# Optimization experiments

Hardware: AMD Instinct MI355X
Metric: run time of the kernel (lower is better)

The kernel has to match this reference:

```python
import math
import jax, jax.numpy as jnp
import numpy as np

N_HEAD = 16
N_EMBD = 1024
HEAD_DIM = N_EMBD // N_HEAD  # 64
SHARED = 16
PRIV = HEAD_DIM - SHARED     # 48
B, T = 4, 2048
STD = 0.02


def setup_inputs() -> dict:
    key = jax.random.key(0)
    ks = jax.random.split(key, 6)
    x = jax.random.normal(ks[0], (B, T, N_EMBD), dtype=jnp.float32)
    # Linear params stored as (in, out); bias zeros per _reset_parameters
    W_share = jax.random.normal(ks[1], (N_EMBD, SHARED), dtype=jnp.float32) * STD
    Wq = jax.random.normal(ks[2], (N_EMBD, N_HEAD * PRIV), dtype=jnp.float32) * STD
    Wk = jax.random.normal(ks[3], (N_EMBD, N_HEAD * PRIV), dtype=jnp.float32) * STD
    Wv = jax.random.normal(ks[4], (N_EMBD, N_EMBD), dtype=jnp.float32) * STD
    Wo = jax.random.normal(ks[5], (N_EMBD, N_EMBD), dtype=jnp.float32) * STD
    return {
        'hidden_states': x,
        'W_share': W_share, 'b_share': jnp.zeros((SHARED,), jnp.float32),
        'Wq': Wq, 'bq': jnp.zeros((N_HEAD * PRIV,), jnp.float32),
        'Wk': Wk, 'bk': jnp.zeros((N_HEAD * PRIV,), jnp.float32),
        'Wv': Wv, 'bv': jnp.zeros((N_EMBD,), jnp.float32),
        'Wo': Wo, 'bo': jnp.zeros((N_EMBD,), jnp.float32),
    }


def reference(hidden_states, W_share, b_share, Wq, bq, Wk, bk, Wv, bv, Wo, bo):
    x = hidden_states
    Bt, Tt, C = x.shape
    # shared projection, broadcast across heads: (B,T,s) -> (B,H,T,s)
    share = x @ W_share + b_share
    share_h = jnp.broadcast_to(share[:, None, :, :], (Bt, N_HEAD, Tt, SHARED))
    # private q/k: (B,T,H*p) -> (B,H,T,p)
    q_priv = (x @ Wq + bq).reshape(Bt, Tt, N_HEAD, PRIV).transpose(0, 2, 1, 3)
    k_priv = (x @ Wk + bk).reshape(Bt, Tt, N_HEAD, PRIV).transpose(0, 2, 1, 3)
    q = jnp.concatenate([share_h, q_priv], axis=-1)  # (B,H,T,head_dim)
    k = jnp.concatenate([share_h, k_priv], axis=-1)
    v = (x @ Wv + bv).reshape(Bt, Tt, N_HEAD, HEAD_DIM).transpose(0, 2, 1, 3)
    scale = 1.0 / math.sqrt(HEAD_DIM)
    att = jnp.einsum('bhqd,bhkd->bhqk', q, k) * scale
    causal = jnp.tril(jnp.ones((Tt, Tt), dtype=bool))
    att = jnp.where(causal[None, None, :, :], att, -jnp.inf)
    att = jax.nn.softmax(att, axis=-1)
    y = jnp.einsum('bhqk,bhkd->bhqd', att, v)
    y = y.transpose(0, 2, 1, 3).reshape(Bt, Tt, C)
    y = y @ Wo + bo
    return y
```

## Files before the change

kernel.cpp:

```cpp
#include <hip/hip_runtime.h>
#include <hip/hip_bf16.h>

typedef unsigned short u16;
typedef short short8 __attribute__((ext_vector_type(8)));
typedef float f32x4 __attribute__((ext_vector_type(4)));

#define N_EMBD   1024
#define N_HEADS  16
#define HEAD_DIM 64
#define PRIV     48
#define SEQ_T    2048
#define BATCH    4
#define M_ROWS   (BATCH*SEQ_T)
#define PNS      2816
#define NTILES   (SEQ_T/64)
#define NT_K     16

#if __has_builtin(__builtin_amdgcn_exp2f)
#define EXP2(x) __builtin_amdgcn_exp2f(x)
#else
#define EXP2(x) exp2f(x)
#endif

#if __has_builtin(__builtin_amdgcn_global_load_lds)
#define HAVE_GLL 1
#else
#define HAVE_GLL 0
#endif

__device__ __forceinline__ u16 f2bf(float f) {
  __hip_bfloat16 h = __float2bfloat16(f);
  return *reinterpret_cast<u16*>(&h);
}
__device__ __forceinline__ float bf2f(u16 s) {
  __hip_bfloat16 h;
  *reinterpret_cast<u16*>(&h) = s;
  return __bfloat162float(h);
}
__device__ __forceinline__ float loadv(const void* p, size_t i, int isf32) {
  return isf32 ? ((const float*)p)[i] : bf2f(((const u16*)p)[i]);
}
__device__ __forceinline__ u16 truncbf(float f) {
  unsigned u = __builtin_bit_cast(unsigned, f);
  return (u16)(u >> 16);
}
#if HAVE_GLL
__device__ __forceinline__ void gload_lds16(const u16* g, u16* l) {
  __builtin_amdgcn_global_load_lds(
      (const __attribute__((address_space(1))) void*)g,
      (__attribute__((address_space(3))) void*)l, 16, 0, 0);
}
#endif

__global__ __launch_bounds__(256) void detect_kernel(const u16* __restrict__ x,
                                                     int* __restrict__ flag) {
  __shared__ int cnt;
  if (threadIdx.x == 0) cnt = 0;
  __syncthreads();
  u16 v = x[2 * threadIdx.x];
  int e = (v >> 7) & 0xFF;
  int junk = (e >= 0xC0 || (e != 0 && e <= 0x30)) ? 1 : 0;
  if (junk) atomicAdd(&cnt, 1);
  __syncthreads();
  if (threadIdx.x == 0) *flag = (cnt > 16) ? 1 : 0;
}

__global__ __launch_bounds__(256) void pack_t_kernel(
    const void* __restrict__ Wsh, const void* __restrict__ Wq,
    const void* __restrict__ Wk,  const void* __restrict__ Wv,
    const void* __restrict__ Wo,
    const void* __restrict__ bsh, const void* __restrict__ bq,
    const void* __restrict__ bk,  const void* __restrict__ bv,
    const void* __restrict__ bo,
    u16* __restrict__ Wcat, u16* __restrict__ Woc,
    u16* __restrict__ bcat, u16* __restrict__ boc,
    const int* __restrict__ flagp)
{
  const int f = *flagp;
  if (blockIdx.z == 5) {
    const int flat = blockIdx.y * 16 + blockIdx.x;
    const int padN = (PNS - 2576) * 1024;
    for (int i = flat * 256 + threadIdx.x; i < padN; i += 256 * 256)
      Wcat[(size_t)2576 * 1024 + i] = 0;
    if (flat == 0) {
      for (int c = threadIdx.x; c < PNS; c += 256) {
        float v = 0.f;
        if (c < 16)        v = loadv(bsh, c, f);
        else if (c < 784)  v = loadv(bq, c - 16, f);
        else if (c < 1552) v = loadv(bk, c - 784, f);
        else if (c < 2576) v = loadv(bv, c - 1552, f);
        bcat[c] = f2bf(v);
      }
    } else if (flat == 1) {
      for (int c = threadIdx.x; c < N_EMBD; c += 256)
        boc[c] = f2bf(loadv(bo, c, f));
    }
    return;
  }
  const void* src; u16* dst; int N, rowOff;
  switch (blockIdx.z) {
    case 0: src = Wsh; dst = Wcat; N = 16;   rowOff = 0;    break;
    case 1: src = Wq;  dst = Wcat; N = 768;  rowOff = 16;   break;
    case 2: src = Wk;  dst = Wcat; N = 768;  rowOff = 784;  break;
    case 3: src = Wv;  dst = Wcat; N = 1024; rowOff = 1552; break;
    default:src = Wo;  dst = Woc;  N = 1024; rowOff = 0;    break;
  }
  const int n0 = blockIdx.x * 64;
  if (n0 >= N) return;
  const int k0 = blockIdx.y * 64;
  __shared__ u16 t[64][65];
  const int tx = threadIdx.x & 63, ty = threadIdx.x >> 6;
#pragma unroll
  for (int rr = 0; rr < 16; rr++) {
    int k = k0 + ty * 16 + rr;
    int n = n0 + tx;
    float v = (n < N) ? loadv(src, (size_t)k * N + n, f) : 0.f;
    t[ty * 16 + rr][tx] = f2bf(v);
  }
  __syncthreads();
#pragma unroll
  for (int rr = 0; rr < 16; rr++) {
    int n = ty * 16 + rr;
    if (n0 + n < N)
      dst[(size_t)(rowOff + n0 + n) * 1024 + k0 + tx] = t[tx][n];
  }
}

__global__ __launch_bounds__(256) void xbf_kernel(const void* __restrict__ x,
                                                  u16* __restrict__ Xb,
                                                  const int* __restrict__ flagp) {
  const int f = *flagp;
  const size_t i = (size_t)blockIdx.x * 256 + threadIdx.x;
  if (f) {
    const float4* p = (const float4*)x;
    float4 a = p[i * 2], b = p[i * 2 + 1];
    u16 t[8] = {f2bf(a.x), f2bf(a.y), f2bf(a.z), f2bf(a.w),
                f2bf(b.x), f2bf(b.y), f2bf(b.z), f2bf(b.w)};
    *(uint4*)&Xb[i * 8] = *(const uint4*)t;
  } else {
    *(uint4*)&Xb[i * 8] = ((const uint4*)x)[i];
  }
}

__global__ __launch_bounds__(512, 2) void gemm8p_kernel(
    const u16* __restrict__ A,
    const u16* __restrict__ Bt,
    const u16* __restrict__ bias,
    void* __restrict__ C, int ldc, int Mtiles,
    const int* __restrict__ flagp, int c_dyn)
{
  __shared__ __align__(16) u16 smem[73728];
  u16* const As = smem;
  u16* const Bs = smem + 3 * 8192;

  const bool cf32 = (c_dyn != 0) && (*flagp != 0);

  const int tid  = threadIdx.x;
  const int lane = tid & 63;
  const int w    = tid >> 6;
  const int quad = lane >> 4, l16 = lane & 15;
  const int wm   = w >> 2, wn = w & 3;

  const int nwg = gridDim.x;
  const int wg  = (blockIdx.x & 7) * (nwg >> 3) + (blockIdx.x >> 3);
  const int mb  = wg % Mtiles, nb = wg / Mtiles;
  const int m0  = mb * 128, n0 = nb * 256;

  int ldsA[2]; size_t glA[2];
  int ldsB[2][2]; size_t glB[2][2];
#pragma unroll
  for (int rd = 0; rd < 2; rd++) {
    int j = tid + rd * 512, rp = j >> 3, s = j & 7;
    int cl = (s ^ (rp & 7)) * 8;
    ldsA[rd] = rp * 64 + s * 8;
    glA[rd]  = (size_t)(m0 + rp) * 1024 + cl;
#pragma unroll
    for (int nh = 0; nh < 2; nh++) {
      int cc = (rp & 31) + nh * 32 + (rp >> 5) * 64;
      ldsB[nh][rd] = cc * 64 + s * 8;
      glB[nh][rd]  = (size_t)(n0 + cc) * 1024 + cl;
    }
  }

#if HAVE_GLL
#define G8(g, l) gload_lds16((g), (l))
#else
#define G8(g, l) (*(uint4*)(l) = *(const uint4*)(g))
#endif
#define STG_A(t, bf)                                                       \
  if ((t) < NT_K) {                                                        \
    _Pragma("unroll") for (int rd = 0; rd < 2; rd++)                       \
      G8(A + glA[rd] + (t) * 64, As + (bf) * 8192 + ldsA[rd]);             \
  }
#define STG_B(nh, t, bf)                                                   \
  if ((t) < NT_K) {                                                        \
    _Pragma("unroll") for (int rd = 0; rd < 2; rd++)                       \
      G8(Bt + glB[nh][rd] + (t) * 64, Bs + (bf) * 16384 + ldsB[nh][rd]);   \
  }

  const int ck0  = ((quad)     ^ (l16 & 7)) * 8;
  const int ck1  = ((4 + quad) ^ (l16 & 7)) * 8;
  const int arow = (wm * 64 + l16) * 64;
  const int brow = (wn * 64 + l16) * 64;

  f32x4 acc[4][4];
#pragma unroll
  for (int i = 0; i < 4; i++)
#pragma unroll
    for (int j = 0; j < 4; j++) acc[i][j] = (f32x4){0.f, 0.f, 0.f, 0.f};

  short8 af[4][2], bA[2][2], bB[2][2];

#define READ_A(cur)                                                        \
  { const u16* pa = As + (cur) * 8192 + arow;                              \
    _Pragma("unroll") for (int m = 0; m < 4; m++) {                        \
      af[m][0] = *(const short8*)(pa + m * 1024 + ck0);                    \
      af[m][1] = *(const short8*)(pa + m * 1024 + ck1); } }
#define READ_B(dst, nh, cur)                                               \
  { const u16* pb = Bs + (cur) * 16384 + brow + (nh) * 2048;               \
    _Pragma("unroll") for (int n = 0; n < 2; n++) {                        \
      dst[n][0] = *(const short8*)(pb + n * 1024 + ck0);                   \
      dst[n][1] = *(const short8*)(pb + n * 1024 + ck1); } }
#define MM16(bfr, nh)                                                      \
  __builtin_amdgcn_s_setprio(1);                                           \
  _Pragma("unroll") for (int m = 0; m < 4; m++)                            \
    _Pragma("unroll") for (int n = 0; n < 2; n++) {                        \
      acc[m][(nh)*2+n] = __builtin_amdgcn_mfma_f32_16x16x32_bf16(          \
          af[m][0], bfr[n][0], acc[m][(nh)*2+n], 0, 0, 0);                 \
      acc[m][(nh)*2+n] = __builtin_amdgcn_mfma_f32_16x16x32_bf16(          \
          af[m][1], bfr[n][1], acc[m][(nh)*2+n], 0, 0, 0); }               \
  __builtin_amdgcn_s_setprio(0);
#define BARR { __builtin_amdgcn_s_barrier(); __builtin_amdgcn_sched_barrier(0); }

  STG_A(0, 0); STG_B(1, 0, 0); STG_B(0, 0, 0);
  STG_A(1, 1); STG_B(1, 1, 1); STG_B(0, 1, 1);
  asm volatile("s_waitcnt vmcnt(6)");
  BARR;

#pragma unroll
  for (int kt = 0; kt < NT_K; kt++) {
    const int cur = kt % 3;
    const int stb = (kt + 2) % 3;
    READ_A(cur); READ_B(bA, 0, cur);
    STG_A(kt + 2, stb); STG_B(1, kt + 2, stb);
    BARR;
    MM16(bA, 0);
    BARR;
    READ_B(bB, 1, cur);
    STG_B(0, kt + 2, stb);
    BARR;
    MM16(bB, 1);
    if (kt < NT_K - 2)       { asm volatile("s_waitcnt vmcnt(6)"); }
    else if (kt == NT_K - 2) { asm volatile("s_waitcnt vmcnt(0)"); }
    BARR;
  }
#undef STG_A
#undef STG_B
#undef READ_A
#undef READ_B
#undef MM16
#undef BARR
#undef G8

  float bvv[4];
#pragma unroll
  for (int ni = 0; ni < 4; ni++)
    bvv[ni] = bf2f(bias[n0 + wn * 64 + ni * 16 + l16]);

  if (!cf32) {
    u16* cs = smem + w * 4096;
#pragma unroll
    for (int m = 0; m < 4; m++)
#pragma unroll
      for (int ni = 0; ni < 4; ni++)
#pragma unroll
        for (int r = 0; r < 4; r++) {
          int row = m * 16 + quad * 4 + r;
          int ch  = ((ni * 2 + (l16 >> 3)) ^ (row & 7)) * 8 + (l16 & 7);
          cs[row * 64 + ch] = f2bf(acc[m][ni][r] + bvv[ni]);
        }
    u16* Cb = (u16*)C;
#pragma unroll
    for (int i = 0; i < 8; i++) {
      int ch = lane + i * 64;
      int rr = ch >> 3, cc = ch & 7;
      short8 v = *(const short8*)(cs + rr * 64 + ((cc ^ (rr & 7)) * 8));
      *(short8*)&Cb[(size_t)(m0 + wm * 64 + rr) * ldc + n0 + wn * 64 + cc * 8] = v;
    }
  } else {
    float* cf = (float*)(void*)smem + w * 2048;
#pragma unroll
    for (int pass = 0; pass < 2; pass++) {
#pragma unroll
      for (int m2 = 0; m2 < 2; m2++)
#pragma unroll
        for (int ni = 0; ni < 4; ni++)
#pragma unroll
          for (int r = 0; r < 4; r++) {
            int row = m2 * 16 + quad * 4 + r;
            int ch  = ((ni * 4 + (l16 >> 2)) ^ (row & 15)) * 4 + (l16 & 3);
            cf[row * 64 + ch] = acc[pass * 2 + m2][ni][r] + bvv[ni];
          }
      float* Cf = (float*)C;
#pragma unroll
      for (int i = 0; i < 8; i++) {
        int ch = lane + i * 64;
        int rr = ch >> 4, cc = ch & 15;
        f32x4 v = *(const f32x4*)(cf + rr * 64 + ((cc ^ (rr & 15)) * 4));
        *(f32x4*)&Cf[(size_t)(m0 + wm * 64 + pass * 32 + rr) * ldc +
                     n0 + wn * 64 + cc * 4] = v;
      }
    }
  }
}

__global__ __launch_bounds__(256) void vt_kernel(const u16* __restrict__ P,
                                                 u16* __restrict__ Vt)
{
  const int tt = blockIdx.x * 64;
  const int bh = blockIdx.y;
  const int b = bh >> 4, h = bh & 15;
  const int vcol = 1552 + h * HEAD_DIM;
  __shared__ u16 t[64][65];
  const int tx = threadIdx.x & 63, ty = threadIdx.x >> 6;
#pragma unroll
  for (int rr = 0; rr < 16; rr++) {
    int r = ty * 16 + rr;
    t[r][tx] = P[((size_t)b * SEQ_T + tt + r) * PNS + vcol + tx];
  }
  __syncthreads();
#pragma unroll
  for (int rr = 0; rr < 16; rr++) {
    int d = ty * 16 + rr;
    Vt[((size_t)bh * 64 + d) * SEQ_T + tt + tx] = t[tx][d];
  }
}

__global__ __launch_bounds__(256, 3) void attn_kernel(
    const u16* __restrict__ P, const u16* __restrict__ Vt,
    u16* __restrict__ Y)
{
  const int bh  = blockIdx.x;
  const int b   = bh >> 4, h = bh & 15;
  const int p   = blockIdx.y;
  const int qtA = p, qtB = NTILES - 1 - p;
  const int tid = threadIdx.x;
  const int w   = tid >> 6;
  const int lane = tid & 63;
  const int quad = lane >> 4, l16 = lane & 15;
  const size_t rowb = (size_t)b * SEQ_T;
  const int qcol = 16 + h * PRIV;
  const int kcol = 784 + h * PRIV;

  __shared__ __align__(16) u16 Ks[2][64 * 64];
  __shared__ __align__(16) u16 Vs[2][64 * 64];
  __shared__ __align__(16) u16 Ps[4][2][16 * 68];

  const float csc = 0.18033688011112042f;
  const int d0  = quad * 8;
  const int cq0 = (d0 < 16) ? d0 : (qcol + d0 - 16);
  const int iA = qtA * 64 + w * 16, iB = qtB * 64 + w * 16;
  const u16* qrowA = P + (rowb + iA + l16) * PNS;
  const u16* qrowB = P + (rowb + iB + l16) * PNS;
  short8 qaA0 = *(const short8*)&qrowA[cq0];
  short8 qaA1 = *(const short8*)&qrowA[qcol + 16 + d0];
  short8 qaB0 = *(const short8*)&qrowB[cq0];
  short8 qaB1 = *(const short8*)&qrowB[qcol + 16 + d0];
#pragma unroll
  for (int e = 0; e < 8; e++) {
    qaA0[e] = (short)f2bf(bf2f((u16)qaA0[e]) * csc);
    qaA1[e] = (short)f2bf(bf2f((u16)qaA1[e]) * csc);
    qaB0[e] = (short)f2bf(bf2f((u16)qaB0[e]) * csc);
    qaB1[e] = (short)f2bf(bf2f((u16)qaB1[e]) * csc);
  }
  short8 ones;
#pragma unroll
  for (int e = 0; e < 8; e++) ones[e] = (short)0x3F80;

#if HAVE_GLL
#define GLOADA(g, l) gload_lds16((g), (l))
#else
#define GLOADA(g, l) (*(uint4*)(l) = *(const uint4*)(g))
#endif
#define STAGE_KV(k0, bb)                                                       \
  {                                                                            \
    _Pragma("unroll") for (int i2 = 0; i2 < 2; i2++) {                         \
      int c   = tid + i2 * 256;                                                \
      int row = c >> 3;                                                        \
      int dg  = ((c & 7) ^ (row & 7)) * 8;                                     \
      int col = (dg < 16) ? dg : (kcol + dg - 16);                             \
      GLOADA(&P[(rowb + (k0) + row) * PNS + col], &Ks[bb][c * 8]);             \
      GLOADA(&Vt[((size_t)bh * 64 + row) * SEQ_T + (k0) + dg], &Vs[bb][c * 8]);\
    }                                                                          \
  }

  f32x4 accyA[4], accyB[4], acclA, acclB;
#pragma unroll
  for (int g = 0; g < 4; g++) {
    accyA[g] = (f32x4){0.f, 0.f, 0.f, 0.f};
    accyB[g] = (f32x4){0.f, 0.f, 0.f, 0.f};
  }
  acclA = (f32x4){0.f, 0.f, 0.f, 0.f};
  acclB = (f32x4){0.f, 0.f, 0.f, 0.f};

  const int nkt = qtB + 1;
  STAGE_KV(0, 0);
  __syncthreads();

  for (int kt = 0; kt < nkt; kt++) {
    const int cur = kt & 1;
    const int k0  = kt * 64;
    if (kt + 1 < nkt) STAGE_KV((kt + 1) * 64, 1 - cur);

    const bool doA = (kt <= qtA);

    float svA[4][4], svB[4][4];
#pragma unroll
    for (int g = 0; g < 4; g++) {
      int j = g * 16 + l16;
      short8 kb0 = *(const short8*)&Ks[cur][j * 64 + ((quad    ) ^ (j & 7)) * 8];
      short8 kb1 = *(const short8*)&Ks[cur][j * 64 + ((quad + 4) ^ (j & 7)) * 8];
      f32x4 sB = (f32x4){0.f, 0.f, 0.f, 0.f};
      sB = __builtin_amdgcn_mfma_f32_16x16x32_bf16(qaB0, kb0, sB, 0, 0, 0);
      sB = __builtin_amdgcn_mfma_f32_16x16x32_bf16(qaB1, kb1, sB, 0, 0, 0);
#pragma unroll
      for (int r = 0; r < 4; r++) svB[g][r] = sB[r];
      if (doA) {
        f32x4 sA = (f32x4){0.f, 0.f, 0.f, 0.f};
        sA = __builtin_amdgcn_mfma_f32_16x16x32_bf16(qaA0, kb0, sA, 0, 0, 0);
        sA = __builtin_amdgcn_mfma_f32_16x16x32_bf16(qaA1, kb1, sA, 0, 0, 0);
#pragma unroll
        for (int r = 0; r < 4; r++) svA[g][r] = sA[r];
      }
    }
    if (kt == qtA && doA) {
#pragma unroll
      for (int g = 0; g < 4; g++)
#pragma unroll
        for (int r = 0; r < 4; r++) {
          int gi = iA + quad * 4 + r;
          int gj = k0 + g * 16 + l16;
          if (gj > gi) svA[g][r] = -__builtin_inff();
        }
    }
    if (kt == qtB) {
#pragma unroll
      for (int g = 0; g < 4; g++)
#pragma unroll
        for (int r = 0; r < 4; r++) {
          int gi = iB + quad * 4 + r;
          int gj = k0 + g * 16 + l16;
          if (gj > gi) svB[g][r] = -__builtin_inff();
        }
    }

    if (doA) {
#pragma unroll
      for (int g = 0; g < 4; g++)
#pragma unroll
        for (int r = 0; r < 4; r++)
          Ps[w][0][(quad * 4 + r) * 68 + g * 16 + l16] = truncbf(EXP2(svA[g][r]));
    }
#pragma unroll
    for (int g = 0; g < 4; g++)
#pragma unroll
      for (int r = 0; r < 4; r++)
        Ps[w][1][(quad * 4 + r) * 68 + g * 16 + l16] = truncbf(EXP2(svB[g][r]));

#pragma unroll
    for (int kf = 0; kf < 2; kf++) {
      short8 vb[4];
#pragma unroll
      for (int g2 = 0; g2 < 4; g2++) {
        int row = g2 * 16 + l16;
        vb[g2] = *(const short8*)&Vs[cur][row * 64 + (((kf * 4 + quad) ^ (row & 7)) * 8)];
      }
      short8 paB = *(const short8*)&Ps[w][1][l16 * 68 + kf * 32 + quad * 8];
      acclB = __builtin_amdgcn_mfma_f32_16x16x32_bf16(paB, ones, acclB, 0, 0, 0);
#pragma unroll
      for (int g2 = 0; g2 < 4; g2++)
        accyB[g2] = __builtin_amdgcn_mfma_f32_16x16x32_bf16(paB, vb[g2], accyB[g2], 0, 0, 0);
      if (doA) {
        short8 paA = *(const short8*)&Ps[w][0][l16 * 68 + kf * 32 + quad * 8];
        acclA = __builtin_amdgcn_mfma_f32_16x16x32_bf16(paA, ones, acclA, 0, 0, 0);
#pragma unroll
        for (int g2 = 0; g2 < 4; g2++)
          accyA[g2] = __builtin_amdgcn_mfma_f32_16x16x32_bf16(paA, vb[g2], accyA[g2], 0, 0, 0);
      }
    }

    if (kt + 1 < nkt) __syncthreads();
  }
#undef STAGE_KV
#undef GLOADA

  float invA[4], invB[4];
#pragma unroll
  for (int r = 0; r < 4; r++) {
    invA[r] = 1.0f / acclA[r];
    invB[r] = 1.0f / acclB[r];
  }
#pragma unroll
  for (int g2 = 0; g2 < 4; g2++) {
    int col = h * HEAD_DIM + g2 * 16 + l16;
#pragma unroll
    for (int r = 0; r < 4; r++) {
      int giA = iA + quad * 4 + r;
      int giB = iB + quad * 4 + r;
      Y[(rowb + giA) * N_EMBD + col] = f2bf(accyA[g2][r] * invA[r]);
      Y[(rowb + giB) * N_EMBD + col] = f2bf(accyB[g2][r] * invB[r]);
    }
  }
}

extern "C" void kernel_launch(void* const* d_in, const int* in_sizes, int n_in,
                              void* d_out, int out_size, void* d_ws, size_t ws_size,
                              hipStream_t stream) {
  (void)in_sizes; (void)n_in; (void)out_size; (void)ws_size;
  const void* x   = d_in[0];
  const void* Wsh = d_in[1];
  const void* bsh = d_in[2];
  const void* Wq  = d_in[3];
  const void* bq  = d_in[4];
  const void* Wk  = d_in[5];
  const void* bk  = d_in[6];
  const void* Wv  = d_in[7];
  const void* bv  = d_in[8];
  const void* Wo  = d_in[9];
  const void* bo  = d_in[10];

  char* wsb = (char*)d_ws;
  int* flag = (int*)wsb;
  u16* ws16 = (u16*)(wsb + 64);
  u16* Wcat = ws16;
  u16* bcat = Wcat + (size_t)PNS * N_EMBD;
  u16* Woc  = bcat + PNS;
  u16* boc  = Woc + (size_t)N_EMBD * N_EMBD;
  u16* Pb   = boc + N_EMBD;
  u16* Yb   = Pb + (size_t)M_ROWS * PNS;
  u16* Vtb  = Yb + (size_t)M_ROWS * N_EMBD;
  u16* Xb   = Yb;

  detect_kernel<<<dim3(1), dim3(256), 0, stream>>>((const u16*)x, flag);
  pack_t_kernel<<<dim3(16, 16, 6), dim3(256), 0, stream>>>(
      Wsh, Wq, Wk, Wv, Wo, bsh, bq, bk, bv, bo, Wcat, Woc, bcat, boc, flag);
  xbf_kernel<<<dim3(M_ROWS * N_EMBD / (256 * 8)), dim3(256), 0, stream>>>(
      x, Xb, flag);
  gemm8p_kernel<<<dim3(64 * (PNS / 256)), dim3(512), 0, stream>>>(
      Xb, Wcat, bcat, Pb, PNS, 64, flag, 0);
  vt_kernel<<<dim3(SEQ_T / 64, BATCH * N_HEADS), dim3(256), 0, stream>>>(
      Pb, Vtb);
  attn_kernel<<<dim3(BATCH * N_HEADS, NTILES / 2), dim3(256), 0, stream>>>(
      Pb, Vtb, Yb);
  gemm8p_kernel<<<dim3(64 * (N_EMBD / 256)), dim3(512), 0, stream>>>(
      Yb, Woc, boc, d_out, N_EMBD, 64, flag, 1);
}
```

Baseline: 291.5 us.

## Shrink attention P staging buffer with XOR swizzle to fit four blocks per CU

After: 345.4 us. 18.5% more time.

```diff
diff --git a/kernel.cpp b/kernel.cpp
--- a/kernel.cpp
+++ b/kernel.cpp
@@ -336,7 +336,7 @@
   }
 }
 
-__global__ __launch_bounds__(256, 3) void attn_kernel(
+__global__ __launch_bounds__(256, 4) void attn_kernel(
     const u16* __restrict__ P, const u16* __restrict__ Vt,
     u16* __restrict__ Y)
 {
@@ -354,7 +354,7 @@
 
   __shared__ __align__(16) u16 Ks[2][64 * 64];
   __shared__ __align__(16) u16 Vs[2][64 * 64];
-  __shared__ __align__(16) u16 Ps[4][2][16 * 68];
+  __shared__ __align__(16) u16 Ps[4][16 * 64];
 
   const float csc = 0.18033688011112042f;
   const int d0  = quad * 8;
@@ -454,34 +454,47 @@
         }
     }
 
-    if (doA) {
-#pragma unroll
-      for (int g = 0; g < 4; g++)
-#pragma unroll
-        for (int r = 0; r < 4; r++)
-          Ps[w][0][(quad * 4 + r) * 68 + g * 16 + l16] = truncbf(EXP2(svA[g][r]));
-    }
 #pragma unroll
     for (int g = 0; g < 4; g++)
 #pragma unroll
-      for (int r = 0; r < 4; r++)
-        Ps[w][1][(quad * 4 + r) * 68 + g * 16 + l16] = truncbf(EXP2(svB[g][r]));
-
+      for (int r = 0; r < 4; r++) {
+        int row = quad * 4 + r;
+        Ps[w][row * 64 + ((g * 2 + (l16 >> 3)) ^ (row & 7)) * 8 + (l16 & 7)] =
+            truncbf(EXP2(svB[g][r]));
+      }
 #pragma unroll
     for (int kf = 0; kf < 2; kf++) {
       short8 vb[4];
 #pragma unroll
       for (int g2 = 0; g2 < 4; g2++) {
-        int row = g2 * 16 + l16;
-        vb[g2] = *(const short8*)&Vs[cur][row * 64 + (((kf * 4 + quad) ^ (row & 7)) * 8)];
+        int rv = g2 * 16 + l16;
+        vb[g2] = *(const short8*)&Vs[cur][rv * 64 + (((kf * 4 + quad) ^ (rv & 7)) * 8)];
       }
-      short8 paB = *(const short8*)&Ps[w][1][l16 * 68 + kf * 32 + quad * 8];
+      short8 paB = *(const short8*)&Ps[w][l16 * 64 + (((kf * 4 + quad) ^ (l16 & 7)) * 8)];
       acclB = __builtin_amdgcn_mfma_f32_16x16x32_bf16(paB, ones, acclB, 0, 0, 0);
 #pragma unroll
       for (int g2 = 0; g2 < 4; g2++)
         accyB[g2] = __builtin_amdgcn_mfma_f32_16x16x32_bf16(paB, vb[g2], accyB[g2], 0, 0, 0);
-      if (doA) {
-        short8 paA = *(const short8*)&Ps[w][0][l16 * 68 + kf * 32 + quad * 8];
+    }
+
+    if (doA) {
+#pragma unroll
+      for (int g = 0; g < 4; g++)
+#pragma unroll
+        for (int r = 0; r < 4; r++) {
+          int row = quad * 4 + r;
+          Ps[w][row * 64 + ((g * 2 + (l16 >> 3)) ^ (row & 7)) * 8 + (l16 & 7)] =
+              truncbf(EXP2(svA[g][r]));
+        }
+#pragma unroll
+      for (int kf = 0; kf < 2; kf++) {
+        short8 vb[4];
+#pragma unroll
+        for (int g2 = 0; g2 < 4; g2++) {
+          int rv = g2 * 16 + l16;
+          vb[g2] = *(const short8*)&Vs[cur][rv * 64 + (((kf * 4 + quad) ^ (rv & 7)) * 8)];
+        }
+        short8 paA = *(const short8*)&Ps[w][l16 * 64 + (((kf * 4 + quad) ^ (l16 & 7)) * 8)];
         acclA = __builtin_amdgcn_mfma_f32_16x16x32_bf16(paA, ones, acclA, 0, 0, 0);
 #pragma unroll
         for (int g2 = 0; g2 < 4; g2++)
```

## Triple-buffer K/V staging with vmcnt-gated barriers and MFMA priority hints

Applied to the files above, without the earlier changes.

Result: faster. 284.0 us (-2.6%).

```diff
diff --git a/kernel.cpp b/kernel.cpp
--- a/kernel.cpp
+++ b/kernel.cpp
@@ -336,7 +336,7 @@
   }
 }
 
-__global__ __launch_bounds__(256, 3) void attn_kernel(
+__global__ __launch_bounds__(256, 2) void attn_kernel(
     const u16* __restrict__ P, const u16* __restrict__ Vt,
     u16* __restrict__ Y)
 {
@@ -352,8 +352,8 @@
   const int qcol = 16 + h * PRIV;
   const int kcol = 784 + h * PRIV;
 
-  __shared__ __align__(16) u16 Ks[2][64 * 64];
-  __shared__ __align__(16) u16 Vs[2][64 * 64];
+  __shared__ __align__(16) u16 Ks[3][64 * 64];
+  __shared__ __align__(16) u16 Vs[3][64 * 64];
   __shared__ __align__(16) u16 Ps[4][2][16 * 68];
 
   const float csc = 0.18033688011112042f;
@@ -377,20 +377,23 @@
 #pragma unroll
   for (int e = 0; e < 8; e++) ones[e] = (short)0x3F80;
 
+  const int nkt = qtB + 1;
+
 #if HAVE_GLL
 #define GLOADA(g, l) gload_lds16((g), (l))
 #else
 #define GLOADA(g, l) (*(uint4*)(l) = *(const uint4*)(g))
 #endif
-#define STAGE_KV(k0, bb)                                                       \
+#define STAGE_KV(t, bb)                                                        \
   {                                                                            \
+    const int kk0 = (t) * 64;                                                  \
     _Pragma("unroll") for (int i2 = 0; i2 < 2; i2++) {                         \
       int c   = tid + i2 * 256;                                                \
       int row = c >> 3;                                                        \
       int dg  = ((c & 7) ^ (row & 7)) * 8;                                     \
       int col = (dg < 16) ? dg : (kcol + dg - 16);                             \
-      GLOADA(&P[(rowb + (k0) + row) * PNS + col], &Ks[bb][c * 8]);             \
-      GLOADA(&Vt[((size_t)bh * 64 + row) * SEQ_T + (k0) + dg], &Vs[bb][c * 8]);\
+      GLOADA(&P[(rowb + kk0 + row) * PNS + col], &Ks[bb][c * 8]);              \
+      GLOADA(&Vt[((size_t)bh * 64 + row) * SEQ_T + kk0 + dg], &Vs[bb][c * 8]); \
     }                                                                          \
   }
 
@@ -403,18 +406,21 @@
   acclA = (f32x4){0.f, 0.f, 0.f, 0.f};
   acclB = (f32x4){0.f, 0.f, 0.f, 0.f};
 
-  const int nkt = qtB + 1;
   STAGE_KV(0, 0);
-  __syncthreads();
+  STAGE_KV(1, 1);
+  asm volatile("s_waitcnt vmcnt(4)" ::: "memory");
+  __builtin_amdgcn_sched_barrier(0);
+  __builtin_amdgcn_s_barrier();
 
   for (int kt = 0; kt < nkt; kt++) {
-    const int cur = kt & 1;
+    const int cur = kt % 3;
     const int k0  = kt * 64;
-    if (kt + 1 < nkt) STAGE_KV((kt + 1) * 64, 1 - cur);
+    if (kt + 2 < nkt) STAGE_KV(kt + 2, (kt + 2) % 3);
 
     const bool doA = (kt <= qtA);
 
     float svA[4][4], svB[4][4];
+    __builtin_amdgcn_s_setprio(1);
 #pragma unroll
     for (int g = 0; g < 4; g++) {
       int j = g * 16 + l16;
@@ -433,6 +439,7 @@
         for (int r = 0; r < 4; r++) svA[g][r] = sA[r];
       }
     }
+    __builtin_amdgcn_s_setprio(0);
     if (kt == qtA && doA) {
 #pragma unroll
       for (int g = 0; g < 4; g++)
@@ -467,6 +474,7 @@
       for (int r = 0; r < 4; r++)
         Ps[w][1][(quad * 4 + r) * 68 + g * 16 + l16] = truncbf(EXP2(svB[g][r]));
 
+    __builtin_amdgcn_s_setprio(1);
 #pragma unroll
     for (int kf = 0; kf < 2; kf++) {
       short8 vb[4];
@@ -488,8 +496,21 @@
           accyA[g2] = __builtin_amdgcn_mfma_f32_16x16x32_bf16(paA, vb[g2], accyA[g2], 0, 0, 0);
       }
     }
-
-    if (kt + 1 < nkt) __syncthreads();
+    __builtin_amdgcn_s_setprio(0);
+
+    if (kt + 3 < nkt) {
+      asm volatile("s_waitcnt vmcnt(4)" ::: "memory");
+      __builtin_amdgcn_sched_barrier(0);
+      __builtin_amdgcn_s_barrier();
+    } else if (kt + 2 == nkt) {
+      asm volatile("s_waitcnt vmcnt(0)" ::: "memory");
+      __builtin_amdgcn_sched_barrier(0);
+      __builtin_amdgcn_s_barrier();
+    } else if (kt + 3 == nkt) {
+      asm volatile("s_waitcnt vmcnt(4)" ::: "memory");
+      __builtin_amdgcn_sched_barrier(0);
+      __builtin_amdgcn_s_barrier();
+    }
   }
 #undef STAGE_KV
 #undef GLOADA
```
